# Kernel tuning notes

Measured on AMD Instinct MI355X. Metric: run time of the kernel, lower is better.

Reference implementation:

```python
import jax, jax.numpy as jnp
import numpy as np

WINDOW = 4
EPS = 1e-5


def setup_inputs() -> dict:
    key = jax.random.key(0)
    ks = jax.random.split(key, 12)
    B, T, D = 2, 4096, 1024
    H = D // 2
    s = 0.02
    return {
        "x": jax.random.normal(ks[0], (B, T, D), dtype=jnp.float32),
        # tension_net: Linear(2D -> D/2), SiLU, Linear(D/2 -> 1). Weights stored [in, out].
        "w1": jax.random.normal(ks[1], (2 * D, H), dtype=jnp.float32) * s,
        "b1": jnp.zeros((H,), dtype=jnp.float32),
        "w2": jax.random.normal(ks[2], (H, 1), dtype=jnp.float32) * s,
        "b2": jnp.zeros((1,), dtype=jnp.float32),
        # wv: Linear(D -> D)
        "wv_w": jax.random.normal(ks[3], (D, D), dtype=jnp.float32) * s,
        "wv_b": jnp.zeros((D,), dtype=jnp.float32),
        # merge: Linear(2D -> D)
        "merge_w": jax.random.normal(ks[4], (2 * D, D), dtype=jnp.float32) * s,
        "merge_b": jnp.zeros((D,), dtype=jnp.float32),
        # LayerNorm(D)
        "gamma": jnp.ones((D,), dtype=jnp.float32),
        "beta": jnp.zeros((D,), dtype=jnp.float32),
    }


def reference(x, w1, b1, w2, b2, wv_w, wv_b, merge_w, merge_b, gamma, beta):
    B, T, D = x.shape
    W = WINDOW
    # Causal sliding-window neighbor gather: nb[:, t, w] = x[:, t-w-1] if t-w-1 >= 0 else 0.
    idx = jnp.arange(T)[:, None] - jnp.arange(W)[None, :] - 1          # [T, W]
    valid = (idx >= 0)                                                  # [T, W]
    nb = jnp.take(x, jnp.clip(idx, 0, None), axis=1)                   # [B, T, W, D]
    nb = jnp.where(valid[None, :, :, None], nb, jnp.zeros((), x.dtype))
    # Pairwise tension gate: tiny MLP on [h_t, nb].
    h_t = jnp.broadcast_to(x[:, :, None, :], (B, T, W, D))
    pair = jnp.concatenate([h_t, nb], axis=-1)                          # [B, T, W, 2D]
    hid = jax.nn.silu(jnp.einsum('btwe,eh->btwh', pair, w1) + b1)       # [B, T, W, D/2]
    tau = jax.nn.sigmoid((jnp.einsum('btwh,ho->btwo', hid, w2) + b2)[..., 0])  # [B, T, W]
    # Value projection of neighbors (note: zero-padded neighbors still get wv bias, matching torch).
    v = jnp.einsum('btwd,de->btwe', nb, wv_w) + wv_b                    # [B, T, W, D]
    msg = jnp.einsum('btw,btwd->btd', tau, v)                           # [B, T, D]
    # Merge + LayerNorm.
    y = jnp.einsum('bte,ed->btd', jnp.concatenate([x, msg], axis=-1), merge_w) + merge_b
    mu = jnp.mean(y, axis=-1, keepdims=True)
    var = jnp.mean(jnp.square(y - mu), axis=-1, keepdims=True)
    y = (y - mu) * jax.lax.rsqrt(var + EPS) * gamma + beta
    return y
```

## Files before the change

### kernel.cpp

```cpp
#include <hip/hip_runtime.h>
#include <hip/hip_bf16.h>

#define TT 4096
#define TD 1024
#define TM 8192
#define CN 3072
#define EPS 1e-5f

typedef __bf16 bf16;
typedef __bf16 bf16x4 __attribute__((ext_vector_type(4)));
typedef __bf16 bf16x8 __attribute__((ext_vector_type(8)));
typedef float  f32x4  __attribute__((ext_vector_type(4)));

#define GLOBAL_AS __attribute__((address_space(1)))
#define LDS_AS    __attribute__((address_space(3)))

__global__ __launch_bounds__(256) void prep_kernel(const float* __restrict__ x,
                                                   const float* __restrict__ w1,
                                                   const float* __restrict__ wv_w,
                                                   const float* __restrict__ wv_b,
                                                   const float* __restrict__ merge_w,
                                                   bf16* __restrict__ Xbf,
                                                   bf16* __restrict__ BigBT,
                                                   bf16* __restrict__ Amb,
                                                   bf16* __restrict__ WvBf,
                                                   float* __restrict__ cvecP) {
    __shared__ float tile[32][33];
    int b = blockIdx.x;
    const int tid = threadIdx.x;

    if (b < 16) {
        const int j = (b & 3) * 256 + tid;
        const int e0 = (b >> 2) * 256;
        const float* col = merge_w + (size_t)(1024 + e0) * 1024 + j;
        float acc = 0.f;
#pragma unroll 32
        for (int e = 0; e < 256; ++e) acc += wv_b[e0 + e] * col[(size_t)e * 1024];
        cvecP[(b >> 2) * 1024 + j] = acc;
        return;
    }
    b -= 16;
    if (b < 8192) {
        int i = b * 256 + tid;
        float4 v = ((const float4*)x)[i];
        bf16x4 o; o[0] = (bf16)v.x; o[1] = (bf16)v.y; o[2] = (bf16)v.z; o[3] = (bf16)v.w;
        *(bf16x4*)(Xbf + (size_t)i * 4) = o;
        return;
    }
    b -= 8192;

    const float* src; bf16* dst; int srcN, tilesX, dstOff;
    if (b < 512)       {            src = w1;                        srcN = 512;  tilesX = 16; dst = BigBT; dstOff = 0;    }
    else if (b < 1024) { b -= 512;  src = w1 + (size_t)1024 * 512;   srcN = 512;  tilesX = 16; dst = BigBT; dstOff = 512;  }
    else if (b < 2048) { b -= 1024; src = merge_w;                   srcN = 1024; tilesX = 32; dst = BigBT; dstOff = 2048; }
    else if (b < 3072) { b -= 2048; src = merge_w + (size_t)1024 * 1024; srcN = 1024; tilesX = 32; dst = Amb; dstOff = 0; }
    else {
        b -= 3072;
        int i = b * 256 + tid;
        float4 v = ((const float4*)wv_w)[i];
        bf16x4 o; o[0] = (bf16)v.x; o[1] = (bf16)v.y; o[2] = (bf16)v.z; o[3] = (bf16)v.w;
        *(bf16x4*)(WvBf + (size_t)i * 4) = o;
        return;
    }
    int n0 = (b % tilesX) * 32, k0 = (b / tilesX) * 32;
    int tx = tid & 31, ty = tid >> 5;
#pragma unroll
    for (int r = 0; r < 32; r += 8)
        tile[ty + r][tx] = src[(size_t)(k0 + ty + r) * srcN + n0 + tx];
    __syncthreads();
#pragma unroll
    for (int r = 0; r < 32; r += 8)
        dst[(size_t)(dstOff + n0 + ty + r) * 1024 + k0 + tx] = (bf16)tile[tx][ty + r];
}

__global__ __launch_bounds__(256) void wprime_kernel(const bf16* __restrict__ Amb,
                                                     const bf16* __restrict__ WvBf,
                                                     bf16* __restrict__ Wout,
                                                     const float* __restrict__ cvecP,
                                                     float* __restrict__ cvec) {
    int b = blockIdx.x;
    if (b == 256) {
        int j = threadIdx.x * 4;
        float4 s0 = *(const float4*)(cvecP + j);
        float4 s1 = *(const float4*)(cvecP + 1024 + j);
        float4 s2 = *(const float4*)(cvecP + 2048 + j);
        float4 s3 = *(const float4*)(cvecP + 3072 + j);
        float4 o = {s0.x + s1.x + s2.x + s3.x, s0.y + s1.y + s2.y + s3.y,
                    s0.z + s1.z + s2.z + s3.z, s0.w + s1.w + s2.w + s3.w};
        *(float4*)(cvec + j) = o;
        return;
    }
    __shared__ bf16 As[64 * 64];
    __shared__ bf16 Bs[64 * 64];
    const int m0 = (b >> 4) * 64;
    const int n0 = (b & 15) * 64;
    const int tid = threadIdx.x;
    const int wave = tid >> 6, lane = tid & 63;
    const int wr = (wave >> 1) * 32, wc = (wave & 1) * 32;
    const int lrow = lane & 15, cbase = lane >> 4;
    const int sw = lrow & 7;

    f32x4 acc[2][2] = {};

    for (int k0 = 0; k0 < 1024; k0 += 64) {
        __syncthreads();
#pragma unroll
        for (int c = 0; c < 2; ++c) {
            int e = (c * 256 + tid) * 8;
            int row = e >> 6;
            int q = (e >> 3) & 7;
            int gcol = ((q ^ (row & 7)) << 3);
            const bf16* ga = Amb  + (size_t)(m0 + row) * 1024 + k0 + gcol;
            const bf16* gb = WvBf + (size_t)(n0 + row) * 1024 + k0 + gcol;
            __builtin_amdgcn_global_load_lds((const GLOBAL_AS void*)ga,
                                             (LDS_AS void*)(As + e), 16, 0, 0);
            __builtin_amdgcn_global_load_lds((const GLOBAL_AS void*)gb,
                                             (LDS_AS void*)(Bs + e), 16, 0, 0);
        }
        __syncthreads();

#pragma unroll
        for (int kk = 0; kk < 2; ++kk) {
            const int qo = ((cbase + kk * 4) ^ sw) << 3;
            bf16x8 af[2], bfr[2];
#pragma unroll
            for (int i = 0; i < 2; ++i) {
                af[i]  = *(const bf16x8*)(As + (wr + i * 16 + lrow) * 64 + qo);
                bfr[i] = *(const bf16x8*)(Bs + (wc + i * 16 + lrow) * 64 + qo);
            }
#pragma unroll
            for (int i = 0; i < 2; ++i)
#pragma unroll
                for (int j = 0; j < 2; ++j)
                    acc[i][j] = __builtin_amdgcn_mfma_f32_16x16x32_bf16(af[i], bfr[j], acc[i][j], 0, 0, 0);
        }
    }

    const int lr = (lane >> 4) * 4, lc = lane & 15;
#pragma unroll
    for (int i = 0; i < 2; ++i)
#pragma unroll
        for (int j = 0; j < 2; ++j)
#pragma unroll
            for (int r = 0; r < 4; ++r)
                Wout[(size_t)(m0 + wr + i * 16 + lr + r) * 1024 + (n0 + wc + j * 16 + lc)]
                    = (bf16)acc[i][j][r];
}

#define MFMA16(a, b, c) __builtin_amdgcn_mfma_f32_16x16x32_bf16((a), (b), (c), 0, 0, 0)

#define STAGE_A(BUF, T) do {                                                      \
    _Pragma("unroll")                                                             \
    for (int ld_ = 0; ld_ < 4; ++ld_) {                                           \
        const bf16* ga_ = aBase + (size_t)(ld_ * 64) * 1024 + (T) * 64;           \
        __builtin_amdgcn_global_load_lds((const GLOBAL_AS void*)ga_,              \
            (LDS_AS void*)(SMEM + (BUF) * 28672 + ld_ * 4096 + tid * 8), 16, 0, 0); \
    } } while (0)

#define STAGE_B(BUF, T) do {                                                      \
    _Pragma("unroll")                                                             \
    for (int ld_ = 0; ld_ < 3; ++ld_) {                                           \
        const bf16* gb_ = bBase + (size_t)(ld_ * 64) * 1024 + (T) * 64;           \
        __builtin_amdgcn_global_load_lds((const GLOBAL_AS void*)gb_,              \
            (LDS_AS void*)(SMEM + (BUF) * 28672 + 16384 + ld_ * 4096 + tid * 8), 16, 0, 0); \
    } } while (0)

#define AF(BUF, I, KK) (*(const bf16x8*)(SMEM + (BUF) * 28672 +                   \
    (wm * 64 + (I) * 16 + lrow) * 64 + (((cbase + (KK) * 4) ^ sw) << 3)))
#define BF(BUF, J, KK) (*(const bf16x8*)(SMEM + (BUF) * 28672 + 16384 +           \
    (wn * 96 + (J) * 16 + lrow) * 64 + (((cbase + (KK) * 4) ^ sw) << 3)))

#define NOSTAGE do {} while (0)
#define NOGATE  do {} while (0)
#define GATE0 do { asm volatile("s_waitcnt vmcnt(0)" ::: "memory");               \
                   __builtin_amdgcn_sched_barrier(0); } while (0)

#define PH(BUF, KK, H, RDB, STAGE, GATE) do {                                     \
    if (RDB) {                                                                    \
        _Pragma("unroll")                                                         \
        for (int j = 0; j < 6; ++j) bfr[j] = BF(BUF, j, KK);                      \
    }                                                                             \
    bf16x8 a0_ = AF(BUF, (H) * 2 + 0, KK);                                        \
    bf16x8 a1_ = AF(BUF, (H) * 2 + 1, KK);                                        \
    STAGE;                                                                        \
    __builtin_amdgcn_s_barrier();                                                 \
    __builtin_amdgcn_sched_barrier(0);                                            \
    __builtin_amdgcn_s_setprio(1);                                                \
    _Pragma("unroll")                                                             \
    for (int j = 0; j < 6; ++j) {                                                 \
        acc[(H) * 2 + 0][j] = MFMA16(a0_, bfr[j], acc[(H) * 2 + 0][j]);           \
        acc[(H) * 2 + 1][j] = MFMA16(a1_, bfr[j], acc[(H) * 2 + 1][j]);           \
    }                                                                             \
    __builtin_amdgcn_s_setprio(0);                                                \
    GATE;                                                                         \
    __builtin_amdgcn_s_barrier();                                                 \
    __builtin_amdgcn_sched_barrier(0);                                            \
} while (0)

#define TILE(BUF, SA, SB, G3)                                                     \
    PH(BUF, 0, 0, 1, SA, NOGATE);                                                 \
    PH(BUF, 0, 1, 0, SB, NOGATE);                                                 \
    PH(BUF, 1, 0, 1, NOSTAGE, NOGATE);                                            \
    PH(BUF, 1, 1, 0, NOSTAGE, G3);

__global__ __launch_bounds__(512, 2) void gemm_big(const bf16* __restrict__ A,
                                                   const bf16* __restrict__ BT,
                                                   bf16* __restrict__ C) {
    __shared__ __align__(16) bf16 SMEM[57344];
    const int NB = 3072, K = 1024;

    const int L = blockIdx.x;
    const int m0 = (L >> 4) * 256;
    const int n0 = ((L & 7) * 2 + ((L >> 3) & 1)) * 192;
    const int tid = threadIdx.x;
    const int wave = tid >> 6, lane = tid & 63;
    const int wm = wave >> 1;
    const int wn = wave & 1;
    const int lrow = lane & 15, cbase = lane >> 4;
    const int sw = lrow & 7;

    const int r0 = tid >> 3;
    const int c0 = ((tid & 7) ^ ((tid >> 3) & 7)) << 3;
    const bf16* aBase = A  + (size_t)(m0 + r0) * K + c0;
    const bf16* bBase = BT + (size_t)(n0 + r0) * K + c0;

    f32x4 acc[4][6] = {};
    bf16x8 bfr[6];

    STAGE_A(0, 0);
    STAGE_B(0, 0);
    asm volatile("s_waitcnt vmcnt(0)" ::: "memory");
    __builtin_amdgcn_sched_barrier(0);
    __builtin_amdgcn_s_barrier();
    __builtin_amdgcn_sched_barrier(0);

    for (int i = 0; i < 7; ++i) {
        const int t1 = 2 * i + 1, t2 = 2 * i + 2;
        TILE(0, STAGE_A(1, t1), STAGE_B(1, t1), GATE0);
        TILE(1, STAGE_A(0, t2), STAGE_B(0, t2), GATE0);
    }
    TILE(0, STAGE_A(1, 15), STAGE_B(1, 15), GATE0);
    TILE(1, NOSTAGE, NOSTAGE, NOGATE);

    __syncthreads();
    bf16* ep = SMEM + wave * 6656;
    const int lr = (lane >> 4) * 4, lc = lane & 15;
#pragma unroll
    for (int i = 0; i < 4; ++i)
#pragma unroll
        for (int j = 0; j < 6; ++j)
#pragma unroll
            for (int r = 0; r < 4; ++r)
                ep[(i * 16 + lr + r) * 104 + (j * 16 + lc)] = (bf16)acc[i][j][r];
    __syncthreads();

    bf16* Cw = C + (size_t)(m0 + wm * 64) * NB + n0 + wn * 96;
#pragma unroll
    for (int p = 0; p < 8; ++p) {
        int R = p * 8 + (lane >> 3);
        int Ccol = (lane & 7) * 8;
        bf16x8 v = *(const bf16x8*)(ep + R * 104 + Ccol);
        *(bf16x8*)(Cw + (size_t)R * NB + Ccol) = v;
    }
#pragma unroll
    for (int p = 0; p < 4; ++p) {
        int R = p * 16 + (lane >> 2);
        int Ccol = 64 + (lane & 3) * 8;
        bf16x8 v = *(const bf16x8*)(ep + R * 104 + Ccol);
        *(bf16x8*)(Cw + (size_t)R * NB + Ccol) = v;
    }
}

__global__ __launch_bounds__(256) void final_kernel(const bf16* __restrict__ C,
                                                    const float* __restrict__ b1,
                                                    const float* __restrict__ b2,
                                                    const float* __restrict__ w2,
                                                    const float* __restrict__ cvec,
                                                    const float* __restrict__ merge_b,
                                                    const float* __restrict__ gamma,
                                                    const float* __restrict__ beta,
                                                    float* __restrict__ out) {
    const int wave = threadIdx.x >> 6, lane = threadIdx.x & 63;
    const int row = blockIdx.x * 4 + wave;
    const int t = row & (TT - 1);
    const bf16* Crow = C + (size_t)row * CN;

    const int h0 = lane * 8;
    bf16x8 u8 = *(const bf16x8*)(Crow + h0);
    float4 b1a = *(const float4*)(b1 + h0), b1b = *(const float4*)(b1 + h0 + 4);
    float4 w2a = *(const float4*)(w2 + h0), w2b = *(const float4*)(w2 + h0 + 4);
    float u[8] = {(float)u8[0] + b1a.x, (float)u8[1] + b1a.y,
                  (float)u8[2] + b1a.z, (float)u8[3] + b1a.w,
                  (float)u8[4] + b1b.x, (float)u8[5] + b1b.y,
                  (float)u8[6] + b1b.z, (float)u8[7] + b1b.w};
    const float w2v[8] = {w2a.x, w2a.y, w2a.z, w2a.w, w2b.x, w2b.y, w2b.z, w2b.w};

    float partial[4];
#pragma unroll
    for (int w = 0; w < 4; ++w) {
        float p = 0.f;
        if (t >= w + 1) {
            bf16x8 v8 = *(const bf16x8*)(C + (size_t)(row - w - 1) * CN + 512 + h0);
#pragma unroll
            for (int k = 0; k < 8; ++k) {
                float z = u[k] + (float)v8[k];
                p += (z / (1.f + __expf(-z))) * w2v[k];
            }
        } else {
#pragma unroll
            for (int k = 0; k < 8; ++k) {
                float z = u[k];
                p += (z / (1.f + __expf(-z))) * w2v[k];
            }
        }
        partial[w] = p;
    }
#pragma unroll
    for (int w = 0; w < 4; ++w)
#pragma unroll
        for (int off = 1; off < 64; off <<= 1)
            partial[w] += __shfl_xor(partial[w], off, 64);

    const float bias2 = b2[0];
    float taus[4];
#pragma unroll
    for (int w = 0; w < 4; ++w)
        taus[w] = 1.f / (1.f + __expf(-(partial[w] + bias2)));
    const float tsum = taus[0] + taus[1] + taus[2] + taus[3];

    const int d0 = lane * 16;
    bf16x8 y1a = *(const bf16x8*)(Crow + 2048 + d0);
    bf16x8 y1b = *(const bf16x8*)(Crow + 2048 + d0 + 8);
    float v[16];
#pragma unroll
    for (int k = 0; k < 8; ++k) { v[k] = (float)y1a[k]; v[8 + k] = (float)y1b[k]; }
#pragma unroll
    for (int q = 0; q < 4; ++q) {
        float4 cv = *(const float4*)(cvec + d0 + q * 4);
        float4 mb = *(const float4*)(merge_b + d0 + q * 4);
        v[q*4+0] += tsum * cv.x + mb.x; v[q*4+1] += tsum * cv.y + mb.y;
        v[q*4+2] += tsum * cv.z + mb.z; v[q*4+3] += tsum * cv.w + mb.w;
    }
#pragma unroll
    for (int w = 0; w < 4; ++w) {
        if (t >= w + 1) {
            const bf16* Pn = C + (size_t)(row - w - 1) * CN + 1024 + d0;
            bf16x8 pa = *(const bf16x8*)Pn;
            bf16x8 pb = *(const bf16x8*)(Pn + 8);
#pragma unroll
            for (int k = 0; k < 8; ++k) {
                v[k] += taus[w] * (float)pa[k];
                v[8 + k] += taus[w] * (float)pb[k];
            }
        }
    }

    float s = 0.f, ss = 0.f;
#pragma unroll
    for (int k = 0; k < 16; ++k) { s += v[k]; ss += v[k] * v[k]; }
#pragma unroll
    for (int off = 1; off < 64; off <<= 1) {
        s  += __shfl_xor(s, off, 64);
        ss += __shfl_xor(ss, off, 64);
    }
    const float mu = s * (1.f / TD);
    const float var = ss * (1.f / TD) - mu * mu;
    const float r = rsqrtf(var + EPS);

#pragma unroll
    for (int q = 0; q < 4; ++q) {
        float4 g  = *(const float4*)(gamma + d0 + q * 4);
        float4 bt = *(const float4*)(beta + d0 + q * 4);
        float4 o;
        o.x = (v[q*4+0] - mu) * r * g.x + bt.x;
        o.y = (v[q*4+1] - mu) * r * g.y + bt.y;
        o.z = (v[q*4+2] - mu) * r * g.z + bt.z;
        o.w = (v[q*4+3] - mu) * r * g.w + bt.w;
        *(float4*)(out + (size_t)row * TD + d0 + q * 4) = o;
    }
}

extern "C" void kernel_launch(void* const* d_in, const int* in_sizes, int n_in,
                              void* d_out, int out_size, void* d_ws, size_t ws_size,
                              hipStream_t stream) {
    const float* x       = (const float*)d_in[0];
    const float* w1      = (const float*)d_in[1];
    const float* b1      = (const float*)d_in[2];
    const float* w2      = (const float*)d_in[3];
    const float* b2      = (const float*)d_in[4];
    const float* wv_w    = (const float*)d_in[5];
    const float* wv_b    = (const float*)d_in[6];
    const float* merge_w = (const float*)d_in[7];
    const float* merge_b = (const float*)d_in[8];
    const float* gamma   = (const float*)d_in[9];
    const float* beta    = (const float*)d_in[10];
    float* out = (float*)d_out;

    char* ws = (char*)d_ws;
    bf16*  Xbf   = (bf16*)ws;  ws += (size_t)TM * 1024 * 2;
    bf16*  BigBT = (bf16*)ws;  ws += (size_t)CN * 1024 * 2;
    bf16*  Amb   = (bf16*)ws;  ws += (size_t)1024 * 1024 * 2;
    bf16*  WvBf  = (bf16*)ws;  ws += (size_t)1024 * 1024 * 2;
    float* cvecP = (float*)ws; ws += (size_t)4 * 1024 * 4;
    float* cvec  = (float*)ws; ws += (size_t)1024 * 4;
    bf16*  Cbuf  = (bf16*)ws;

    prep_kernel<<<12304, 256, 0, stream>>>(x, w1, wv_w, wv_b, merge_w,
                                           Xbf, BigBT, Amb, WvBf, cvecP);

    wprime_kernel<<<257, 256, 0, stream>>>(Amb, WvBf, BigBT + (size_t)1024 * 1024,
                                           cvecP, cvec);

    gemm_big<<<512, 512, 0, stream>>>(Xbf, BigBT, Cbuf);

    final_kernel<<<TM / 4, 256, 0, stream>>>(Cbuf, b1, b2, w2, cvec, merge_b,
                                             gamma, beta, out);
}
```

Measured before the change: 198.8 us.

## Deepen GEMM prefetch to two tiles ahead with partial vmcnt waits

The big bf16 GEMM now issues loads two K-tiles ahead instead of one. Each buffer is refilled right after the barrier in the last phase that reads it, and the wait drops from a full vmcnt(0) drain to vmcnt(7), so the next tile's seven loads stay in flight across the barrier. This is meant to hide more global-to-LDS latency behind MFMA work. It relies on the vmcnt accounting and barrier placement being exact, because an error would be a silent data race.

```diff
diff --git a/kernel.cpp b/kernel.cpp
--- a/kernel.cpp
+++ b/kernel.cpp
@@ -149,15 +149,13 @@
 
 #define MFMA16(a, b, c) __builtin_amdgcn_mfma_f32_16x16x32_bf16((a), (b), (c), 0, 0, 0)
 
-#define STAGE_A(BUF, T) do {                                                      \
+#define STAGE_AB(BUF, T) do {                                                     \
     _Pragma("unroll")                                                             \
     for (int ld_ = 0; ld_ < 4; ++ld_) {                                           \
         const bf16* ga_ = aBase + (size_t)(ld_ * 64) * 1024 + (T) * 64;           \
         __builtin_amdgcn_global_load_lds((const GLOBAL_AS void*)ga_,              \
             (LDS_AS void*)(SMEM + (BUF) * 28672 + ld_ * 4096 + tid * 8), 16, 0, 0); \
-    } } while (0)
-
-#define STAGE_B(BUF, T) do {                                                      \
+    }                                                                             \
     _Pragma("unroll")                                                             \
     for (int ld_ = 0; ld_ < 3; ++ld_) {                                           \
         const bf16* gb_ = bBase + (size_t)(ld_ * 64) * 1024 + (T) * 64;           \
@@ -172,19 +170,21 @@
 
 #define NOSTAGE do {} while (0)
 #define NOGATE  do {} while (0)
+#define GATE7 do { asm volatile("s_waitcnt vmcnt(7)" ::: "memory");               \
+                   __builtin_amdgcn_sched_barrier(0); } while (0)
 #define GATE0 do { asm volatile("s_waitcnt vmcnt(0)" ::: "memory");               \
                    __builtin_amdgcn_sched_barrier(0); } while (0)
 
-#define PH(BUF, KK, H, RDB, STAGE, GATE) do {                                     \
+#define PH(BUF, KK, H, RDB, SPOST, GATE) do {                                     \
     if (RDB) {                                                                    \
         _Pragma("unroll")                                                         \
         for (int j = 0; j < 6; ++j) bfr[j] = BF(BUF, j, KK);                      \
     }                                                                             \
     bf16x8 a0_ = AF(BUF, (H) * 2 + 0, KK);                                        \
     bf16x8 a1_ = AF(BUF, (H) * 2 + 1, KK);                                        \
-    STAGE;                                                                        \
     __builtin_amdgcn_s_barrier();                                                 \
     __builtin_amdgcn_sched_barrier(0);                                            \
+    SPOST;                                                                        \
     __builtin_amdgcn_s_setprio(1);                                                \
     _Pragma("unroll")                                                             \
     for (int j = 0; j < 6; ++j) {                                                 \
@@ -197,11 +197,11 @@
     __builtin_amdgcn_sched_barrier(0);                                            \
 } while (0)
 
-#define TILE(BUF, SA, SB, G3)                                                     \
-    PH(BUF, 0, 0, 1, SA, NOGATE);                                                 \
-    PH(BUF, 0, 1, 0, SB, NOGATE);                                                 \
+#define TILE(BUF, SP3, G3)                                                        \
+    PH(BUF, 0, 0, 1, NOSTAGE, NOGATE);                                            \
+    PH(BUF, 0, 1, 0, NOSTAGE, NOGATE);                                            \
     PH(BUF, 1, 0, 1, NOSTAGE, NOGATE);                                            \
-    PH(BUF, 1, 1, 0, NOSTAGE, G3);
+    PH(BUF, 1, 1, 0, SP3, G3);
 
 __global__ __launch_bounds__(512, 2) void gemm_big(const bf16* __restrict__ A,
                                                    const bf16* __restrict__ BT,
@@ -227,20 +227,20 @@
     f32x4 acc[4][6] = {};
     bf16x8 bfr[6];
 
-    STAGE_A(0, 0);
-    STAGE_B(0, 0);
-    asm volatile("s_waitcnt vmcnt(0)" ::: "memory");
+    STAGE_AB(0, 0);
+    STAGE_AB(1, 1);
+    asm volatile("s_waitcnt vmcnt(7)" ::: "memory");
     __builtin_amdgcn_sched_barrier(0);
     __builtin_amdgcn_s_barrier();
     __builtin_amdgcn_sched_barrier(0);
 
     for (int i = 0; i < 7; ++i) {
-        const int t1 = 2 * i + 1, t2 = 2 * i + 2;
-        TILE(0, STAGE_A(1, t1), STAGE_B(1, t1), GATE0);
-        TILE(1, STAGE_A(0, t2), STAGE_B(0, t2), GATE0);
-    }
-    TILE(0, STAGE_A(1, 15), STAGE_B(1, 15), GATE0);
-    TILE(1, NOSTAGE, NOSTAGE, NOGATE);
+        const int t2 = 2 * i + 2, t3 = 2 * i + 3;
+        TILE(0, STAGE_AB(0, t2), GATE7);
+        TILE(1, STAGE_AB(1, t3), GATE7);
+    }
+    TILE(0, NOSTAGE, GATE0);
+    TILE(1, NOSTAGE, NOGATE);
 
     __syncthreads();
     bf16* ep = SMEM + wave * 6656;
```

Measured after the change: 199.3 us. Within noise of the previous version (+0.2%).

## Replace ping-pong phased GEMM schedule with simple per-K-tile double buffering

Applied to the files above, without the earlier changes.

The big GEMM drops its four-phase-per-tile schedule, which used interleaved barriers, setprio and staged A/B loads split across phases. Each K-tile now issues all async loads for the next buffer up front, runs the full 4x6 MFMA block over both k-steps, then waits and synchronises once. The launch bound moves from 2 to 1 blocks per CU, which lets the compiler use more registers. The aim is to cut barrier overhead, but it gives up the wave ping-pong overlap and likely some occupancy.

```diff
diff --git a/kernel.cpp b/kernel.cpp
--- a/kernel.cpp
+++ b/kernel.cpp
@@ -149,15 +149,13 @@
 
 #define MFMA16(a, b, c) __builtin_amdgcn_mfma_f32_16x16x32_bf16((a), (b), (c), 0, 0, 0)
 
-#define STAGE_A(BUF, T) do {                                                      \
+#define STAGE_AB(BUF, T) do {                                                     \
     _Pragma("unroll")                                                             \
     for (int ld_ = 0; ld_ < 4; ++ld_) {                                           \
         const bf16* ga_ = aBase + (size_t)(ld_ * 64) * 1024 + (T) * 64;           \
         __builtin_amdgcn_global_load_lds((const GLOBAL_AS void*)ga_,              \
             (LDS_AS void*)(SMEM + (BUF) * 28672 + ld_ * 4096 + tid * 8), 16, 0, 0); \
-    } } while (0)
-
-#define STAGE_B(BUF, T) do {                                                      \
+    }                                                                             \
     _Pragma("unroll")                                                             \
     for (int ld_ = 0; ld_ < 3; ++ld_) {                                           \
         const bf16* gb_ = bBase + (size_t)(ld_ * 64) * 1024 + (T) * 64;           \
@@ -171,39 +169,29 @@
     (wn * 96 + (J) * 16 + lrow) * 64 + (((cbase + (KK) * 4) ^ sw) << 3)))
 
 #define NOSTAGE do {} while (0)
-#define NOGATE  do {} while (0)
-#define GATE0 do { asm volatile("s_waitcnt vmcnt(0)" ::: "memory");               \
-                   __builtin_amdgcn_sched_barrier(0); } while (0)
-
-#define PH(BUF, KK, H, RDB, STAGE, GATE) do {                                     \
-    if (RDB) {                                                                    \
+
+#define KTILE(BUF, STAGE_STMT) do {                                               \
+    STAGE_STMT;                                                                   \
+    _Pragma("unroll")                                                             \
+    for (int kk = 0; kk < 2; ++kk) {                                              \
+        bf16x8 bfr[6];                                                            \
         _Pragma("unroll")                                                         \
-        for (int j = 0; j < 6; ++j) bfr[j] = BF(BUF, j, KK);                      \
+        for (int j = 0; j < 6; ++j) bfr[j] = BF(BUF, j, kk);                      \
+        _Pragma("unroll")                                                         \
+        for (int i = 0; i < 4; ++i) {                                             \
+            bf16x8 a_ = AF(BUF, i, kk);                                           \
+            _Pragma("unroll")                                                     \
+            for (int j = 0; j < 6; ++j)                                           \
+                acc[i][j] = MFMA16(a_, bfr[j], acc[i][j]);                        \
+        }                                                                         \
     }                                                                             \
-    bf16x8 a0_ = AF(BUF, (H) * 2 + 0, KK);                                        \
-    bf16x8 a1_ = AF(BUF, (H) * 2 + 1, KK);                                        \
-    STAGE;                                                                        \
-    __builtin_amdgcn_s_barrier();                                                 \
+    asm volatile("s_waitcnt vmcnt(0)" ::: "memory");                              \
     __builtin_amdgcn_sched_barrier(0);                                            \
-    __builtin_amdgcn_s_setprio(1);                                                \
-    _Pragma("unroll")                                                             \
-    for (int j = 0; j < 6; ++j) {                                                 \
-        acc[(H) * 2 + 0][j] = MFMA16(a0_, bfr[j], acc[(H) * 2 + 0][j]);           \
-        acc[(H) * 2 + 1][j] = MFMA16(a1_, bfr[j], acc[(H) * 2 + 1][j]);           \
-    }                                                                             \
-    __builtin_amdgcn_s_setprio(0);                                                \
-    GATE;                                                                         \
     __builtin_amdgcn_s_barrier();                                                 \
     __builtin_amdgcn_sched_barrier(0);                                            \
 } while (0)
 
-#define TILE(BUF, SA, SB, G3)                                                     \
-    PH(BUF, 0, 0, 1, SA, NOGATE);                                                 \
-    PH(BUF, 0, 1, 0, SB, NOGATE);                                                 \
-    PH(BUF, 1, 0, 1, NOSTAGE, NOGATE);                                            \
-    PH(BUF, 1, 1, 0, NOSTAGE, G3);
-
-__global__ __launch_bounds__(512, 2) void gemm_big(const bf16* __restrict__ A,
+__global__ __launch_bounds__(512, 1) void gemm_big(const bf16* __restrict__ A,
                                                    const bf16* __restrict__ BT,
                                                    bf16* __restrict__ C) {
     __shared__ __align__(16) bf16 SMEM[57344];
@@ -225,10 +213,8 @@
     const bf16* bBase = BT + (size_t)(n0 + r0) * K + c0;
 
     f32x4 acc[4][6] = {};
-    bf16x8 bfr[6];
-
-    STAGE_A(0, 0);
-    STAGE_B(0, 0);
+
+    STAGE_AB(0, 0);
     asm volatile("s_waitcnt vmcnt(0)" ::: "memory");
     __builtin_amdgcn_sched_barrier(0);
     __builtin_amdgcn_s_barrier();
@@ -236,11 +222,11 @@
 
     for (int i = 0; i < 7; ++i) {
         const int t1 = 2 * i + 1, t2 = 2 * i + 2;
-        TILE(0, STAGE_A(1, t1), STAGE_B(1, t1), GATE0);
-        TILE(1, STAGE_A(0, t2), STAGE_B(0, t2), GATE0);
-    }
-    TILE(0, STAGE_A(1, 15), STAGE_B(1, 15), GATE0);
-    TILE(1, NOSTAGE, NOSTAGE, NOGATE);
+        KTILE(0, STAGE_AB(1, t1));
+        KTILE(1, STAGE_AB(0, t2));
+    }
+    KTILE(0, STAGE_AB(1, 15));
+    KTILE(1, NOSTAGE);
 
     __syncthreads();
     bf16* ep = SMEM + wave * 6656;
```

New measurement: 200.9 us. About the same (+1.0%).
